# Kernel optimization log

Measured on AMD Instinct MI355X. Metric: run time of the kernel, lower is better.

The kernel has to match this reference:

```python
import jax, jax.numpy as jnp
import numpy as np

TAU = 1.0
L = -0.1
R = 1.1
COUPLING_K = 2.0
EPS = 1e-6
LN_EPS = 1e-5


def entmax15(x, axis=-1):
    # Peters & Martins alpha=1.5 entmax via sort + threshold search.
    x = x / 2.0
    x = x - jnp.max(x, axis=axis, keepdims=True)
    xs = jnp.flip(jnp.sort(x, axis=axis), axis=axis)  # descending
    k = x.shape[axis]
    rho = jnp.arange(1, k + 1, dtype=x.dtype)
    mean = jnp.cumsum(xs, axis=axis) / rho
    mean_sq = jnp.cumsum(xs * xs, axis=axis) / rho
    ss = rho * (mean_sq - mean * mean)
    delta = jnp.clip((1.0 - ss) / rho, 0.0, None)
    tau = mean - jnp.sqrt(delta)
    support_size = jnp.sum(tau <= xs, axis=axis, keepdims=True)
    tau_star = jnp.take_along_axis(tau, support_size - 1, axis=axis)
    y = jnp.clip(x - tau_star, 0.0, None)
    return y * y


def setup_inputs() -> dict:
    key = jax.random.key(0)
    ks = jax.random.split(key, 4)
    B, S, D, H = 32, 4096, 768, 1024
    return {
        "embeddings": jax.random.normal(ks[0], (B, S, D), dtype=jnp.float32),
        "attn": jnp.ones((B, S), dtype=jnp.float32),
        "u": jax.random.uniform(ks[1], (B, S), dtype=jnp.float32),
        "ln_g": jnp.ones((D,), dtype=jnp.float32),
        "ln_b": jnp.zeros((D,), dtype=jnp.float32),
        "w1": jax.random.normal(ks[2], (H, D), dtype=jnp.float32) * 0.02,
        "b1": jnp.zeros((H,), dtype=jnp.float32),
        "w2": jax.random.normal(ks[3], (1, H), dtype=jnp.float32) * 0.02,
        "b2": jnp.zeros((1,), dtype=jnp.float32),
    }


def reference(embeddings, attn, u, ln_g, ln_b, w1, b1, w2, b2):
    # mask embeddings
    emb = embeddings * attn[..., None]                       # [B,S,D]
    # LayerNorm
    mu = jnp.mean(emb, axis=-1, keepdims=True)
    var = jnp.mean((emb - mu) ** 2, axis=-1, keepdims=True)
    x = (emb - mu) / jnp.sqrt(var + LN_EPS) * ln_g + ln_b
    # MLP scorer (dropout = identity in eval)
    h1 = jax.nn.gelu(jnp.einsum("bsd,hd->bsh", x, w1) + b1, approximate=False)
    scores = (jnp.einsum("bsh,oh->bso", h1, w2) + b2)[..., 0]  # [B,S]
    scores = jnp.where(attn == 0, -1e9, scores)
    # sparse attention over sequence axis
    z = entmax15(scores / TAU, axis=1) * attn
    # Kumaraswamy relaxed sampling with coupling
    eff = scores + COUPLING_K * (2.0 * z - 1.0)
    a = jax.nn.softplus(eff) + EPS
    b = jax.nn.softplus(-eff) + EPS
    uc = jnp.clip(u, EPS, 1.0 - EPS)
    xk = (1.0 - (1.0 - uc) ** (1.0 / b)) ** (1.0 / a)
    y = L + (R - L) * xk
    h = (jnp.clip(y, 0.0, 1.0) > 0.5).astype(scores.dtype) * attn
    # straight-through gate
    g = jax.lax.stop_gradient(h - z) + z
    reg = jnp.zeros((), dtype=scores.dtype)
    return (z, g, reg)
```

## Files before the change

### kernel.cpp

```cpp
#include <hip/hip_runtime.h>
#include <math.h>

#define NB 32
#define NS 4096
#define ND 768
#define NH 1024
#define NTOK (NB*NS)
#define NKC (ND/32)

typedef __bf16 bf16_t;
typedef __bf16 bf16x8 __attribute__((ext_vector_type(8)));
typedef float  f32x4  __attribute__((ext_vector_type(4)));

__global__ __launch_bounds__(256) void k_lnstats(
    const float* __restrict__ emb, const float* __restrict__ attn,
    float* __restrict__ mu_o, float* __restrict__ rs_o)
{
    const int token = blockIdx.x * 4 + (threadIdx.x >> 6);
    const int lane  = threadIdx.x & 63;
    const float am  = attn[token];
    const float* row = emb + (size_t)token * ND;

    float e[12];
    {
        const float4 v0 = *(const float4*)(row + lane * 4);
        const float4 v1 = *(const float4*)(row + 256 + lane * 4);
        const float4 v2 = *(const float4*)(row + 512 + lane * 4);
        e[0]=v0.x; e[1]=v0.y; e[2]=v0.z; e[3]=v0.w;
        e[4]=v1.x; e[5]=v1.y; e[6]=v1.z; e[7]=v1.w;
        e[8]=v2.x; e[9]=v2.y; e[10]=v2.z; e[11]=v2.w;
    }
    float s = 0.f;
#pragma unroll
    for (int j = 0; j < 12; j++) { e[j] *= am; s += e[j]; }
#pragma unroll
    for (int m = 32; m; m >>= 1) s += __shfl_xor(s, m, 64);
    const float mu = s * (1.0f / ND);

    float v = 0.f;
#pragma unroll
    for (int j = 0; j < 12; j++) { float d = e[j] - mu; v += d * d; }
#pragma unroll
    for (int m = 32; m; m >>= 1) v += __shfl_xor(v, m, 64);
    v *= (1.0f / ND);

    if (lane == 0) {
        mu_o[token] = mu;
        rs_o[token] = (float)(1.0 / sqrt((double)v + 1e-5));
    }
}

__global__ __launch_bounds__(256) void k_wprep(
    const float* __restrict__ w1, bf16_t* __restrict__ whB, bf16_t* __restrict__ wlB)
{
    const int t   = blockIdx.x * 256 + threadIdx.x;
    const int ln  = t & 63;
    const int h16 = (t >> 6) & 63;
    const int c   = t >> 12;
    const int row = h16 * 16 + (ln >> 2);
    const int k0  = c * 32 + 8 * ((ln & 3) ^ (ln >> 4));

    const float4 a = *(const float4*)(w1 + (size_t)row * ND + k0);
    const float4 b = *(const float4*)(w1 + (size_t)row * ND + k0 + 4);
    const float vv[8] = {a.x,a.y,a.z,a.w,b.x,b.y,b.z,b.w};
    bf16x8 hi, lo;
#pragma unroll
    for (int j = 0; j < 8; j++) {
        const bf16_t hj = (bf16_t)vv[j];
        hi[j] = hj;
        lo[j] = (bf16_t)(vv[j] - (float)hj);
    }
    const size_t o = (size_t)t * 8;
    *(bf16x8*)(whB + o) = hi;
    *(bf16x8*)(wlB + o) = lo;
}

#define TM 64
#define KC 32

__global__ __launch_bounds__(256, 2) void k_scorer(
    const float* __restrict__ emb, const float* __restrict__ attn,
    const float* __restrict__ ln_g, const float* __restrict__ ln_b,
    const bf16_t* __restrict__ whB, const bf16_t* __restrict__ wlB,
    const float* __restrict__ b1, const float* __restrict__ w2,
    const float* __restrict__ b2v,
    const float* __restrict__ mu_a, const float* __restrict__ rs_a,
    float* __restrict__ scores)
{
    __shared__ __align__(16) bf16_t sWh[2][256*32];
    __shared__ __align__(16) bf16_t sWl[2][256*32];
    __shared__ __align__(16) bf16_t sXh[64*32];
    __shared__ __align__(16) bf16_t sXl[64*32];
    __shared__ float sred[4*64];

    const int tid    = threadIdx.x;
    const int lane   = tid & 63;
    const int wv     = tid >> 6;
    const int token0 = blockIdx.x * TM;

    const int xt  = tid >> 2;
    const int xp  = tid & 3;
    const int xk8 = 8 * (xp ^ ((xt >> 2) & 3));
    const float x_mu = mu_a[token0 + xt];
    const float x_rs = rs_a[token0 + xt];
    const float x_at = attn[token0 + xt];
    const float* embrow = emb + (size_t)(token0 + xt) * ND;

    const int cn  = lane & 15;
    const int cq  = lane >> 4;
    const int fsw = (cq ^ (cn >> 2)) << 3;

    f32x4 acc[4][4];
    float spart[16];
#pragma unroll
    for (int i = 0; i < 16; i++) spart[i] = 0.f;

    float4 xe0, xe1, xg0, xg1, xb0, xb1;

    auto loadX = [&](int c) {
        const int kc = c * KC;
        xe0 = *(const float4*)(embrow + kc + xk8);
        xe1 = *(const float4*)(embrow + kc + xk8 + 4);
        xg0 = *(const float4*)(ln_g + kc + xk8);
        xg1 = *(const float4*)(ln_g + kc + xk8 + 4);
        xb0 = *(const float4*)(ln_b + kc + xk8);
        xb1 = *(const float4*)(ln_b + kc + xk8 + 4);
    };
    auto storeX = [&]() {
        const float ev[8] = {xe0.x,xe0.y,xe0.z,xe0.w,xe1.x,xe1.y,xe1.z,xe1.w};
        const float gv[8] = {xg0.x,xg0.y,xg0.z,xg0.w,xg1.x,xg1.y,xg1.z,xg1.w};
        const float cv[8] = {xb0.x,xb0.y,xb0.z,xb0.w,xb1.x,xb1.y,xb1.z,xb1.w};
        bf16x8 hi, lo;
#pragma unroll
        for (int j = 0; j < 8; j++) {
            const float x = (ev[j] * x_at - x_mu) * x_rs * gv[j] + cv[j];
            const bf16_t hb = (bf16_t)x;
            hi[j] = hb;
            lo[j] = (bf16_t)(x - (float)hb);
        }
        *(bf16x8*)&sXh[xt*32 + xp*8] = hi;
        *(bf16x8*)&sXl[xt*32 + xp*8] = lo;
    };
    auto issueW = [&](int hq, int c, int buf) {
        const size_t blk = ((size_t)(c * 64 + hq * 16 + wv * 4)) * 512 + lane * 8;
        const bf16_t* gh = whB + blk;
        const bf16_t* gl = wlB + blk;
#pragma unroll
        for (int i = 0; i < 4; i++)
            __builtin_amdgcn_global_load_lds(
                (const __attribute__((address_space(1))) void*)(gh + i * 512),
                (__attribute__((address_space(3))) void*)&sWh[buf][(wv*64 + i*16)*32],
                16, 0, 0);
#pragma unroll
        for (int i = 0; i < 4; i++)
            __builtin_amdgcn_global_load_lds(
                (const __attribute__((address_space(1))) void*)(gl + i * 512),
                (__attribute__((address_space(3))) void*)&sWl[buf][(wv*64 + i*16)*32],
                16, 0, 0);
    };

    loadX(0);
    issueW(0, 0, 0);
    storeX();
    __syncthreads();

    int cur = 0;
    for (int hq = 0; hq < 4; hq++) {
#pragma unroll
        for (int tt = 0; tt < 4; tt++)
#pragma unroll
            for (int ht = 0; ht < 4; ht++) acc[tt][ht] = (f32x4){0.f, 0.f, 0.f, 0.f};

        for (int c = 0; c < 24; c++) {
            const bool lastiter = (hq == 3) && (c == 23);
            if (!lastiter) {
                const int nhq = (c == 23) ? hq + 1 : hq;
                const int nc  = (c == 23) ? 0 : c + 1;
                loadX(nc);
                issueW(nhq, nc, cur ^ 1);
            }
            bf16x8 ah[4], al[4];
#pragma unroll
            for (int tt = 0; tt < 4; tt++) {
                const int off = (tt*16 + cn)*32 + fsw;
                ah[tt] = *(const bf16x8*)&sXh[off];
                al[tt] = *(const bf16x8*)&sXl[off];
            }
#pragma unroll
            for (int ht = 0; ht < 4; ht++) {
                const int off = (wv*64 + ht*16 + cn)*32 + fsw;
                const bf16x8 bh = *(const bf16x8*)&sWh[cur][off];
                const bf16x8 bl = *(const bf16x8*)&sWl[cur][off];
#pragma unroll
                for (int tt = 0; tt < 4; tt++) {
                    acc[tt][ht] = __builtin_amdgcn_mfma_f32_16x16x32_bf16(ah[tt], bh, acc[tt][ht], 0, 0, 0);
                    acc[tt][ht] = __builtin_amdgcn_mfma_f32_16x16x32_bf16(al[tt], bh, acc[tt][ht], 0, 0, 0);
                    acc[tt][ht] = __builtin_amdgcn_mfma_f32_16x16x32_bf16(ah[tt], bl, acc[tt][ht], 0, 0, 0);
                }
            }
            __syncthreads();
            if (!lastiter) storeX();
            __syncthreads();
            cur ^= 1;
        }
#pragma unroll
        for (int ht = 0; ht < 4; ht++) {
            const int hg = hq*256 + wv*64 + ht*16 + cn;
            const float b1v = b1[hg];
            const float w2v = w2[hg];
#pragma unroll
            for (int tt = 0; tt < 4; tt++)
#pragma unroll
                for (int r = 0; r < 4; r++) {
                    const float pre = acc[tt][ht][r] + b1v;
                    const float ge  = 0.5f * pre * (1.0f + erff(pre * 0.70710678118654752f));
                    spart[tt*4 + r] += ge * w2v;
                }
        }
    }
#pragma unroll
    for (int i = 0; i < 16; i++) {
        float s = spart[i];
        s += __shfl_xor(s, 1, 64);
        s += __shfl_xor(s, 2, 64);
        s += __shfl_xor(s, 4, 64);
        s += __shfl_xor(s, 8, 64);
        spart[i] = s;
    }
    if (cn == 0) {
#pragma unroll
        for (int tt = 0; tt < 4; tt++)
#pragma unroll
            for (int r = 0; r < 4; r++)
                sred[wv*64 + tt*16 + cq*4 + r] = spart[tt*4 + r];
    }
    __syncthreads();
    if (tid < TM) {
        scores[token0 + tid] = sred[tid] + sred[64 + tid] + sred[128 + tid] + sred[192 + tid] + b2v[0];
    }
}

static __device__ __forceinline__ double softplus_d(double x) {
    return (x > 30.0) ? x : log1p(exp(x));
}

__global__ __launch_bounds__(1024) void k_taugate(
    const float* __restrict__ scores, const float* __restrict__ attn,
    const float* __restrict__ u, float* __restrict__ out)
{
    const int b    = blockIdx.x;
    const int tid  = threadIdx.x;
    const int lane = tid & 63;
    const int wid  = tid >> 6;

    __shared__ double redd[2][16];
    __shared__ float  redf[16];
    __shared__ float  bcf;

    float vv[4], at[4], sm[4];
#pragma unroll
    for (int j = 0; j < 4; j++) {
        const int i = tid + 1024 * j;
        at[j] = attn[b * NS + i];
        const float s = scores[b * NS + i];
        sm[j] = (at[j] == 0.0f) ? -1e9f : s;
        vv[j] = sm[j] * 0.5f;
    }

    float mx = fmaxf(fmaxf(vv[0], vv[1]), fmaxf(vv[2], vv[3]));
#pragma unroll
    for (int m = 32; m; m >>= 1) mx = fmaxf(mx, __shfl_xor(mx, m, 64));
    if (lane == 0) redf[wid] = mx;
    __syncthreads();
    if (tid == 0) {
        float t = redf[0];
        for (int i = 1; i < 16; i++) t = fmaxf(t, redf[i]);
        bcf = t;
    }
    __syncthreads();
    const double mxd = (double)bcf;

    double d[4];
#pragma unroll
    for (int j = 0; j < 4; j++) d[j] = (double)vv[j] - mxd;

    double lo = -1.0, hi = 0.0;
    for (int it = 0; it < 44; it++) {
        const double mid = 0.5 * (lo + hi);
        double s = 0.0;
#pragma unroll
        for (int j = 0; j < 4; j++) {
            const double t = d[j] - mid;
            if (t > 0.0) s += t * t;
        }
#pragma unroll
        for (int m = 32; m; m >>= 1) s += __shfl_xor(s, m, 64);
        const int p = it & 1;
        if (lane == 0) redd[p][wid] = s;
        __syncthreads();
        double tot = 0.0;
#pragma unroll
        for (int i = 0; i < 16; i++) tot += redd[p][i];
        if (tot >= 1.0) lo = mid; else hi = mid;
    }
    const double tau = lo;

    if (b == 0 && tid == 0) out[2 * NTOK] = 0.0f;

#pragma unroll
    for (int j = 0; j < 4; j++) {
        const int i = tid + 1024 * j;
        const double t  = d[j] - tau;
        const double zz = (t > 0.0) ? t * t : 0.0;
        const float  z  = (float)zz * at[j];

        const double eff  = (double)sm[j] + 2.0 * (2.0 * (double)z - 1.0);
        const double sp_p = softplus_d(eff)  + 1e-6;
        const double sp_n = softplus_d(-eff) + 1e-6;
        const double uc   = fmin(fmax((double)u[b * NS + i], 1e-6), 1.0 - 1e-6);
        const double xk   = pow(1.0 - pow(1.0 - uc, 1.0 / sp_n), 1.0 / sp_p);
        const double y    = -0.1 + 1.2 * xk;
        const double ycl  = fmin(fmax(y, 0.0), 1.0);
        float h = (ycl > 0.5) ? 1.0f : 0.0f;
        h *= at[j];
        const float g = (h - z) + z;

        out[b * NS + i]        = z;
        out[NTOK + b * NS + i] = g;
    }
}

extern "C" void kernel_launch(void* const* d_in, const int* in_sizes, int n_in,
                              void* d_out, int out_size, void* d_ws, size_t ws_size,
                              hipStream_t stream)
{
    const float* emb  = (const float*)d_in[0];
    const float* attn = (const float*)d_in[1];
    const float* u    = (const float*)d_in[2];
    const float* ln_g = (const float*)d_in[3];
    const float* ln_b = (const float*)d_in[4];
    const float* w1   = (const float*)d_in[5];
    const float* b1   = (const float*)d_in[6];
    const float* w2   = (const float*)d_in[7];
    const float* b2   = (const float*)d_in[8];
    float* out = (float*)d_out;

    float*  wsf    = (float*)d_ws;
    float*  scores = wsf;
    float*  mu     = wsf + NTOK;
    float*  rs     = wsf + 2 * NTOK;
    bf16_t* w1hB   = (bf16_t*)(wsf + 3 * NTOK);
    bf16_t* w1lB   = w1hB + (size_t)NH * ND;

    hipLaunchKernelGGL(k_lnstats, dim3(NTOK / 4), dim3(256), 0, stream,
                       emb, attn, mu, rs);
    hipLaunchKernelGGL(k_wprep, dim3((NKC * 64 * 64) / 256), dim3(256), 0, stream,
                       w1, w1hB, w1lB);
    hipLaunchKernelGGL(k_scorer, dim3(NTOK / TM), dim3(256), 0, stream,
                       emb, attn, ln_g, ln_b, w1hB, w1lB, b1, w2, b2, mu, rs, scores);
    hipLaunchKernelGGL(k_taugate, dim3(NB), dim3(1024), 0, stream,
                       scores, attn, u, out);
}
```

Measured before the change: 1.365 ms.

## Enlarge scorer tile to 256 tokens with 8 waves and double-buffered X

New measurement: 1.629 ms. +19.4%, slower.

```diff
diff --git a/kernel.cpp b/kernel.cpp
--- a/kernel.cpp
+++ b/kernel.cpp
@@ -75,10 +75,10 @@
     *(bf16x8*)(wlB + o) = lo;
 }
 
-#define TM 64
+#define TM 256
 #define KC 32
 
-__global__ __launch_bounds__(256, 2) void k_scorer(
+__global__ __launch_bounds__(512, 2) void k_scorer(
     const float* __restrict__ emb, const float* __restrict__ attn,
     const float* __restrict__ ln_g, const float* __restrict__ ln_b,
     const bf16_t* __restrict__ whB, const bf16_t* __restrict__ wlB,
@@ -89,18 +89,22 @@
 {
     __shared__ __align__(16) bf16_t sWh[2][256*32];
     __shared__ __align__(16) bf16_t sWl[2][256*32];
-    __shared__ __align__(16) bf16_t sXh[64*32];
-    __shared__ __align__(16) bf16_t sXl[64*32];
-    __shared__ float sred[4*64];
+    __shared__ __align__(16) bf16_t sXh[2][256*32];
+    __shared__ __align__(16) bf16_t sXl[2][256*32];
+    __shared__ float sred[2][256];
 
     const int tid    = threadIdx.x;
     const int lane   = tid & 63;
     const int wv     = tid >> 6;
+    const int wt     = wv >> 1;
+    const int wh     = wv & 1;
     const int token0 = blockIdx.x * TM;
 
-    const int xt  = tid >> 2;
-    const int xp  = tid & 3;
-    const int xk8 = 8 * (xp ^ ((xt >> 2) & 3));
+    const int xt  = tid >> 1;
+    const int xp  = tid & 1;
+    const int xm  = (xt >> 2) & 3;
+    const int sl0 = (xp * 2 + 0) ^ xm;
+    const int sl1 = (xp * 2 + 1) ^ xm;
     const float x_mu = mu_a[token0 + xt];
     const float x_rs = rs_a[token0 + xt];
     const float x_at = attn[token0 + xt];
@@ -110,58 +114,77 @@
     const int cq  = lane >> 4;
     const int fsw = (cq ^ (cn >> 2)) << 3;
 
-    f32x4 acc[4][4];
+    f32x4 acc[4][8];
     float spart[16];
 #pragma unroll
     for (int i = 0; i < 16; i++) spart[i] = 0.f;
 
-    float4 xe0, xe1, xg0, xg1, xb0, xb1;
+    float4 xe0, xe1, xe2, xe3;
+    int xkc = 0;
 
     auto loadX = [&](int c) {
-        const int kc = c * KC;
-        xe0 = *(const float4*)(embrow + kc + xk8);
-        xe1 = *(const float4*)(embrow + kc + xk8 + 4);
-        xg0 = *(const float4*)(ln_g + kc + xk8);
-        xg1 = *(const float4*)(ln_g + kc + xk8 + 4);
-        xb0 = *(const float4*)(ln_b + kc + xk8);
-        xb1 = *(const float4*)(ln_b + kc + xk8 + 4);
+        xkc = c * KC;
+        xe0 = *(const float4*)(embrow + xkc + 8 * sl0);
+        xe1 = *(const float4*)(embrow + xkc + 8 * sl0 + 4);
+        xe2 = *(const float4*)(embrow + xkc + 8 * sl1);
+        xe3 = *(const float4*)(embrow + xkc + 8 * sl1 + 4);
     };
-    auto storeX = [&]() {
-        const float ev[8] = {xe0.x,xe0.y,xe0.z,xe0.w,xe1.x,xe1.y,xe1.z,xe1.w};
-        const float gv[8] = {xg0.x,xg0.y,xg0.z,xg0.w,xg1.x,xg1.y,xg1.z,xg1.w};
-        const float cv[8] = {xb0.x,xb0.y,xb0.z,xb0.w,xb1.x,xb1.y,xb1.z,xb1.w};
-        bf16x8 hi, lo;
-#pragma unroll
-        for (int j = 0; j < 8; j++) {
-            const float x = (ev[j] * x_at - x_mu) * x_rs * gv[j] + cv[j];
-            const bf16_t hb = (bf16_t)x;
-            hi[j] = hb;
-            lo[j] = (bf16_t)(x - (float)hb);
-        }
-        *(bf16x8*)&sXh[xt*32 + xp*8] = hi;
-        *(bf16x8*)&sXl[xt*32 + xp*8] = lo;
+    auto storeX = [&](int buf) {
+        const float4 g0 = *(const float4*)(ln_g + xkc + 8 * sl0);
+        const float4 g1 = *(const float4*)(ln_g + xkc + 8 * sl0 + 4);
+        const float4 c0 = *(const float4*)(ln_b + xkc + 8 * sl0);
+        const float4 c1 = *(const float4*)(ln_b + xkc + 8 * sl0 + 4);
+        const float4 g2 = *(const float4*)(ln_g + xkc + 8 * sl1);
+        const float4 g3 = *(const float4*)(ln_g + xkc + 8 * sl1 + 4);
+        const float4 c2 = *(const float4*)(ln_b + xkc + 8 * sl1);
+        const float4 c3 = *(const float4*)(ln_b + xkc + 8 * sl1 + 4);
+        {
+            const float ev[8] = {xe0.x,xe0.y,xe0.z,xe0.w,xe1.x,xe1.y,xe1.z,xe1.w};
+            const float gv[8] = {g0.x,g0.y,g0.z,g0.w,g1.x,g1.y,g1.z,g1.w};
+            const float cv[8] = {c0.x,c0.y,c0.z,c0.w,c1.x,c1.y,c1.z,c1.w};
+            bf16x8 hi, lo;
+#pragma unroll
+            for (int j = 0; j < 8; j++) {
+                const float x = (ev[j] * x_at - x_mu) * x_rs * gv[j] + cv[j];
+                const bf16_t hb = (bf16_t)x;
+                hi[j] = hb;
+                lo[j] = (bf16_t)(x - (float)hb);
+            }
+            *(bf16x8*)&sXh[buf][xt*32 + (xp*2 + 0)*8] = hi;
+            *(bf16x8*)&sXl[buf][xt*32 + (xp*2 + 0)*8] = lo;
+        }
+        {
+            const float ev[8] = {xe2.x,xe2.y,xe2.z,xe2.w,xe3.x,xe3.y,xe3.z,xe3.w};
+            const float gv[8] = {g2.x,g2.y,g2.z,g2.w,g3.x,g3.y,g3.z,g3.w};
+            const float cv[8] = {c2.x,c2.y,c2.z,c2.w,c3.x,c3.y,c3.z,c3.w};
+            bf16x8 hi, lo;
+#pragma unroll
+            for (int j = 0; j < 8; j++) {
+                const float x = (ev[j] * x_at - x_mu) * x_rs * gv[j] + cv[j];
+                const bf16_t hb = (bf16_t)x;
+                hi[j] = hb;
+                lo[j] = (bf16_t)(x - (float)hb);
+            }
+            *(bf16x8*)&sXh[buf][xt*32 + (xp*2 + 1)*8] = hi;
+            *(bf16x8*)&sXl[buf][xt*32 + (xp*2 + 1)*8] = lo;
+        }
     };
     auto issueW = [&](int hq, int c, int buf) {
-        const size_t blk = ((size_t)(c * 64 + hq * 16 + wv * 4)) * 512 + lane * 8;
-        const bf16_t* gh = whB + blk;
-        const bf16_t* gl = wlB + blk;
+        const int grp4 = wv >> 1;
+        const bf16_t* gsrc = (wv & 1) ? wlB : whB;
+        bf16_t* lbase = (wv & 1) ? &sWl[buf][0] : &sWh[buf][0];
+        const size_t blk = ((size_t)(c * 64 + hq * 16 + grp4 * 4)) * 512 + lane * 8;
 #pragma unroll
         for (int i = 0; i < 4; i++)
             __builtin_amdgcn_global_load_lds(
-                (const __attribute__((address_space(1))) void*)(gh + i * 512),
-                (__attribute__((address_space(3))) void*)&sWh[buf][(wv*64 + i*16)*32],
-                16, 0, 0);
-#pragma unroll
-        for (int i = 0; i < 4; i++)
-            __builtin_amdgcn_global_load_lds(
-                (const __attribute__((address_space(1))) void*)(gl + i * 512),
-                (__attribute__((address_space(3))) void*)&sWl[buf][(wv*64 + i*16)*32],
+                (const __attribute__((address_space(1))) void*)(gsrc + blk + (size_t)i * 512),
+                (__attribute__((address_space(3))) void*)(lbase + (grp4*64 + i*16)*32),
                 16, 0, 0);
     };
 
     loadX(0);
     issueW(0, 0, 0);
-    storeX();
+    storeX(0);
     __syncthreads();
 
     int cur = 0;
@@ -169,7 +192,7 @@
 #pragma unroll
         for (int tt = 0; tt < 4; tt++)
 #pragma unroll
-            for (int ht = 0; ht < 4; ht++) acc[tt][ht] = (f32x4){0.f, 0.f, 0.f, 0.f};
+            for (int ht = 0; ht < 8; ht++) acc[tt][ht] = (f32x4){0.f, 0.f, 0.f, 0.f};
 
         for (int c = 0; c < 24; c++) {
             const bool lastiter = (hq == 3) && (c == 23);
@@ -182,13 +205,13 @@
             bf16x8 ah[4], al[4];
 #pragma unroll
             for (int tt = 0; tt < 4; tt++) {
-                const int off = (tt*16 + cn)*32 + fsw;
-                ah[tt] = *(const bf16x8*)&sXh[off];
-                al[tt] = *(const bf16x8*)&sXl[off];
-            }
-#pragma unroll
-            for (int ht = 0; ht < 4; ht++) {
-                const int off = (wv*64 + ht*16 + cn)*32 + fsw;
+                const int off = (wt*64 + tt*16 + cn)*32 + fsw;
+                ah[tt] = *(const bf16x8*)&sXh[cur][off];
+                al[tt] = *(const bf16x8*)&sXl[cur][off];
+            }
+#pragma unroll
+            for (int ht = 0; ht < 8; ht++) {
+                const int off = (wh*128 + ht*16 + cn)*32 + fsw;
                 const bf16x8 bh = *(const bf16x8*)&sWh[cur][off];
                 const bf16x8 bl = *(const bf16x8*)&sWl[cur][off];
 #pragma unroll
@@ -198,14 +221,13 @@
                     acc[tt][ht] = __builtin_amdgcn_mfma_f32_16x16x32_bf16(ah[tt], bl, acc[tt][ht], 0, 0, 0);
                 }
             }
-            __syncthreads();
-            if (!lastiter) storeX();
+            if (!lastiter) storeX(cur ^ 1);
             __syncthreads();
             cur ^= 1;
         }
 #pragma unroll
-        for (int ht = 0; ht < 4; ht++) {
-            const int hg = hq*256 + wv*64 + ht*16 + cn;
+        for (int ht = 0; ht < 8; ht++) {
+            const int hg = hq*256 + wh*128 + ht*16 + cn;
             const float b1v = b1[hg];
             const float w2v = w2[hg];
 #pragma unroll
@@ -232,11 +254,11 @@
         for (int tt = 0; tt < 4; tt++)
 #pragma unroll
             for (int r = 0; r < 4; r++)
-                sred[wv*64 + tt*16 + cq*4 + r] = spart[tt*4 + r];
+                sred[wh][wt*64 + tt*16 + cq*4 + r] = spart[tt*4 + r];
     }
     __syncthreads();
     if (tid < TM) {
-        scores[token0 + tid] = sred[tid] + sred[64 + tid] + sred[128 + tid] + sred[192 + tid] + b2v[0];
+        scores[token0 + tid] = sred[0][tid] + sred[1][tid] + b2v[0];
     }
 }
 
@@ -356,7 +378,7 @@
                        emb, attn, mu, rs);
     hipLaunchKernelGGL(k_wprep, dim3((NKC * 64 * 64) / 256), dim3(256), 0, stream,
                        w1, w1hB, w1lB);
-    hipLaunchKernelGGL(k_scorer, dim3(NTOK / TM), dim3(256), 0, stream,
+    hipLaunchKernelGGL(k_scorer, dim3(NTOK / TM), dim3(512), 0, stream,
                        emb, attn, ln_g, ln_b, w1hB, w1lB, b1, w2, b2, mu, rs, scores);
     hipLaunchKernelGGL(k_taugate, dim3(NB), dim3(1024), 0, stream,
                        scores, attn, u, out);
```
